# Optimization experiments

Hardware: AMD Instinct MI355X
Metric: run time of the kernel (lower is better)

Reference implementation:

```python
import jax, jax.numpy as jnp
import numpy as np

CH_IN = 128
HD = 128
HEADS = 4
INNER = HD * HEADS  # 512
N_POINTS = 32768
K = 16
BN_EPS = 1e-5


def setup_inputs() -> dict:
    key = jax.random.key(0)
    ks = jax.random.split(key, 8)
    s = CH_IN ** -0.5
    return {
        "h": jax.random.normal(ks[0], (N_POINTS, K, CH_IN), dtype=jnp.float32),
        "x": jax.random.normal(ks[1], (N_POINTS, CH_IN), dtype=jnp.float32),
        "Wq": jax.random.normal(ks[2], (CH_IN, INNER), dtype=jnp.float32) * s,
        "Wk": jax.random.normal(ks[3], (CH_IN, INNER), dtype=jnp.float32) * s,
        "Wv": jax.random.normal(ks[4], (CH_IN, INNER), dtype=jnp.float32) * s,
        "Wo": jax.random.normal(ks[5], (INNER, CH_IN), dtype=jnp.float32) * (INNER ** -0.5),
        "bo": jnp.zeros((CH_IN,), dtype=jnp.float32),
        "gamma": jnp.ones((HD,), dtype=jnp.float32),
        "beta": jnp.zeros((HD,), dtype=jnp.float32),
    }


def reference(h, x, Wq, Wk, Wv, Wo, bo, gamma, beta):
    n, k, c = h.shape
    scale = c ** -0.5
    # QKV projections (no bias)
    q = (x @ Wq).reshape(n, HEADS, HD)                    # [n,h,d]
    kk = (h @ Wk).reshape(n, k, HEADS, HD)                # [n,K,h,d]
    v = (h @ Wv).reshape(n, k, HEADS, HD)                 # [n,K,h,d]
    # per-point attention scores over K neighbors
    scores = jnp.einsum('nkhd,nhd->nhk', kk, q) * scale   # [n,h,K]
    # FAITHFUL: torch softmax is over a trailing singleton dim -> all ones
    w = jax.nn.softmax(scores[..., None], axis=-1)[..., 0]  # [n,h,K] == 1
    out = jnp.einsum('nkhd,nhk->nhd', v, w).reshape(n, INNER)
    # output projection
    out = out @ Wo + bo                                   # [n, ch_in]
    # BatchNorm1d (training-mode batch stats, biased variance)
    mu = out.mean(axis=0)
    var = out.var(axis=0)
    out = (out - mu) * jax.lax.rsqrt(var + BN_EPS) * gamma + beta
    # ReLU (dropout in eval mode = identity)
    return jax.nn.relu(out)
```

## Files before the change

kernel.cpp:

```cpp
#include <hip/hip_runtime.h>

#define NPTS  32768
#define KNB   16
#define CH    128
#define INNER 512
#define EPS   1e-5f

#define WS_M     0
#define WS_STATS 16384

typedef float f4 __attribute__((ext_vector_type(4)));

__global__ __launch_bounds__(256) void k_wvwo(const float* __restrict__ Wv,
                                              const float* __restrict__ Wo,
                                              float* __restrict__ M,
                                              float* __restrict__ stats) {
    int t  = threadIdx.x;
    if (blockIdx.x == 0) stats[t] = 0.f;
    int id = blockIdx.x * 256 + t;
    int c  = id >> 7;
    int cp = id & 127;
    const float* wvr = Wv + c * INNER;
    float a0 = 0.f, a1 = 0.f, a2 = 0.f, a3 = 0.f;
#pragma unroll 4
    for (int i = 0; i < INNER; i += 4) {
        a0 = fmaf(wvr[i + 0], Wo[(i + 0) * CH + cp], a0);
        a1 = fmaf(wvr[i + 1], Wo[(i + 1) * CH + cp], a1);
        a2 = fmaf(wvr[i + 2], Wo[(i + 2) * CH + cp], a2);
        a3 = fmaf(wvr[i + 3], Wo[(i + 3) * CH + cp], a3);
    }
    M[c * CH + cp] = (a0 + a1) + (a2 + a3);
}

__global__ __launch_bounds__(256) void k_main(const float* __restrict__ h,
                                              const float* __restrict__ Mg,
                                              float* __restrict__ y,
                                              float* __restrict__ stats) {
    __shared__ f4    hs4[32 * 32];
    __shared__ float red[4][2][128];

    const int t  = threadIdx.x;
    const int n0 = blockIdx.x * 32;
    const f4* __restrict__ h4 = (const f4*)h;

#pragma unroll 2
    for (int j = 0; j < 4; ++j) {
        int pi = t + 256 * j;
        int p  = pi >> 5;
        int c4 = pi & 31;
        size_t base = (size_t)(n0 + p) * (KNB * 32) + c4;
        f4 a = __builtin_nontemporal_load(&h4[base]);
#pragma unroll
        for (int k = 1; k < KNB; ++k) {
            f4 v = __builtin_nontemporal_load(&h4[base + (size_t)k * 32]);
            a += v;
        }
        hs4[p * 32 + c4] = a;
    }
    __syncthreads();

    const int w  = t >> 6;
    const int l  = t & 63;
    const int p0 = w * 8;
    float acc0[8] = {0,0,0,0,0,0,0,0};
    float acc1[8] = {0,0,0,0,0,0,0,0};

    for (int cc = 0; cc < 32; ++cc) {
        const int c = 4 * cc;
        float m00 = Mg[(c + 0) * CH + l];
        float m01 = Mg[(c + 1) * CH + l];
        float m02 = Mg[(c + 2) * CH + l];
        float m03 = Mg[(c + 3) * CH + l];
        float m10 = Mg[(c + 0) * CH + 64 + l];
        float m11 = Mg[(c + 1) * CH + 64 + l];
        float m12 = Mg[(c + 2) * CH + 64 + l];
        float m13 = Mg[(c + 3) * CH + 64 + l];
#pragma unroll
        for (int p = 0; p < 8; ++p) {
            f4 hv = hs4[(p0 + p) * 32 + cc];
            acc0[p] = fmaf(hv.x, m00, acc0[p]);
            acc0[p] = fmaf(hv.y, m01, acc0[p]);
            acc0[p] = fmaf(hv.z, m02, acc0[p]);
            acc0[p] = fmaf(hv.w, m03, acc0[p]);
            acc1[p] = fmaf(hv.x, m10, acc1[p]);
            acc1[p] = fmaf(hv.y, m11, acc1[p]);
            acc1[p] = fmaf(hv.z, m12, acc1[p]);
            acc1[p] = fmaf(hv.w, m13, acc1[p]);
        }
    }

    float s0 = 0.f, s1 = 0.f, q0 = 0.f, q1 = 0.f;
#pragma unroll
    for (int p = 0; p < 8; ++p) {
        size_t row = (size_t)(n0 + p0 + p) * CH;
        y[row + l]      = acc0[p];
        y[row + 64 + l] = acc1[p];
        s0 += acc0[p];  q0 = fmaf(acc0[p], acc0[p], q0);
        s1 += acc1[p];  q1 = fmaf(acc1[p], acc1[p], q1);
    }
    red[w][0][l]      = s0;
    red[w][0][64 + l] = s1;
    red[w][1][l]      = q0;
    red[w][1][64 + l] = q1;
    __syncthreads();
    {
        int s = t >> 7, c = t & 127;
        float v = red[0][s][c] + red[1][s][c] + red[2][s][c] + red[3][s][c];
        atomicAdd(&stats[t], v);
    }
}

__global__ __launch_bounds__(256) void k_norm(float* __restrict__ y,
                                              const float* __restrict__ stats,
                                              const float* __restrict__ gamma,
                                              const float* __restrict__ beta) {
    __shared__ float sa[128], sb[128];
    int t = threadIdx.x;
    if (t < 128) {
        float S  = stats[t];
        float Q  = stats[128 + t];
        float mu = S * (1.f / NPTS);
        float var = Q * (1.f / NPTS) - mu * mu;
        float a  = gamma[t] * rsqrtf(var + EPS);
        sa[t] = a;
        sb[t] = beta[t] - mu * a;
    }
    __syncthreads();

    int gid = blockIdx.x * 256 + t;
    f4* y4 = (f4*)y;
    int c0 = (gid & 31) * 4;
    f4 a = { sa[c0], sa[c0 + 1], sa[c0 + 2], sa[c0 + 3] };
    f4 b = { sb[c0], sb[c0 + 1], sb[c0 + 2], sb[c0 + 3] };
#pragma unroll
    for (int i = 0; i < 4; ++i) {
        size_t idx = (size_t)gid + (size_t)i * 262144;
        f4 v = y4[idx];
        v.x = fmaxf(0.f, fmaf(v.x, a.x, b.x));
        v.y = fmaxf(0.f, fmaf(v.y, a.y, b.y));
        v.z = fmaxf(0.f, fmaf(v.z, a.z, b.z));
        v.w = fmaxf(0.f, fmaf(v.w, a.w, b.w));
        y4[idx] = v;
    }
}

extern "C" void kernel_launch(void* const* d_in, const int* in_sizes, int n_in,
                              void* d_out, int out_size, void* d_ws, size_t ws_size,
                              hipStream_t stream) {
    const float* h     = (const float*)d_in[0];
    const float* Wv    = (const float*)d_in[4];
    const float* Wo    = (const float*)d_in[5];
    const float* gamma = (const float*)d_in[7];
    const float* beta  = (const float*)d_in[8];

    float* out   = (float*)d_out;
    float* ws    = (float*)d_ws;
    float* M     = ws + WS_M;
    float* stats = ws + WS_STATS;

    k_wvwo<<<64,   256, 0, stream>>>(Wv, Wo, M, stats);
    k_main<<<1024, 256, 0, stream>>>(h, M, out, stats);
    k_norm<<<1024, 256, 0, stream>>>(out, stats, gamma, beta);
}
```

Before: 412.7 us.

## Fuse projection and BatchNorm into one cooperative kernel with grid sync

Replaces the separate main and normalize kernels with one cooperative kernel of 512 blocks, each handling 64 points. Each block keeps its outputs in registers across a grid-wide sync, then applies BatchNorm and ReLU and writes the final values once. This removes the write-then-reread of the intermediate output and one kernel launch. The costs are a grid barrier, higher register pressure from 32 accumulators per thread, and a dependency on all 512 blocks being co-resident; if the cooperative launch fails, the code falls back to the old two-kernel path.

Measured after the change: 452.5 us. +9.6%, slower.

```diff
diff --git a/kernel.cpp b/kernel.cpp
--- a/kernel.cpp
+++ b/kernel.cpp
@@ -1,10 +1,15 @@
 #include <hip/hip_runtime.h>
+#include <hip/hip_cooperative_groups.h>
+
+namespace cg = cooperative_groups;
 
 #define NPTS  32768
 #define KNB   16
 #define CH    128
 #define INNER 512
 #define EPS   1e-5f
+#define PPB   64
+#define NBLK  (NPTS / PPB)
 
 #define WS_M     0
 #define WS_STATS 16384
@@ -32,6 +37,110 @@
     M[c * CH + cp] = (a0 + a1) + (a2 + a3);
 }
 
+__global__ __launch_bounds__(256, 2) void k_fused(const float* __restrict__ h,
+                                                  const float* __restrict__ Mg,
+                                                  float* __restrict__ y,
+                                                  float* __restrict__ stats,
+                                                  const float* __restrict__ gamma,
+                                                  const float* __restrict__ beta) {
+    __shared__ f4    hs4[PPB * 32];
+    __shared__ float red[4][2][128];
+    __shared__ float sa[128], sb[128];
+
+    const int t  = threadIdx.x;
+    const int n0 = blockIdx.x * PPB;
+    const f4* __restrict__ h4 = (const f4*)h;
+
+#pragma unroll 2
+    for (int j = 0; j < 8; ++j) {
+        int pi = t + 256 * j;
+        int p  = pi >> 5;
+        int c4 = pi & 31;
+        size_t base = (size_t)(n0 + p) * (KNB * 32) + c4;
+        f4 a = __builtin_nontemporal_load(&h4[base]);
+#pragma unroll
+        for (int k = 1; k < KNB; ++k) {
+            f4 v = __builtin_nontemporal_load(&h4[base + (size_t)k * 32]);
+            a += v;
+        }
+        hs4[p * 32 + c4] = a;
+    }
+    __syncthreads();
+
+    const int w  = t >> 6;
+    const int l  = t & 63;
+    const int p0 = w * 16;
+    float acc0[16], acc1[16];
+#pragma unroll
+    for (int p = 0; p < 16; ++p) { acc0[p] = 0.f; acc1[p] = 0.f; }
+
+    for (int cc = 0; cc < 32; ++cc) {
+        const int c = 4 * cc;
+        float m00 = Mg[(c + 0) * CH + l];
+        float m01 = Mg[(c + 1) * CH + l];
+        float m02 = Mg[(c + 2) * CH + l];
+        float m03 = Mg[(c + 3) * CH + l];
+        float m10 = Mg[(c + 0) * CH + 64 + l];
+        float m11 = Mg[(c + 1) * CH + 64 + l];
+        float m12 = Mg[(c + 2) * CH + 64 + l];
+        float m13 = Mg[(c + 3) * CH + 64 + l];
+#pragma unroll
+        for (int p = 0; p < 16; ++p) {
+            f4 hv = hs4[(p0 + p) * 32 + cc];
+            acc0[p] = fmaf(hv.x, m00, acc0[p]);
+            acc0[p] = fmaf(hv.y, m01, acc0[p]);
+            acc0[p] = fmaf(hv.z, m02, acc0[p]);
+            acc0[p] = fmaf(hv.w, m03, acc0[p]);
+            acc1[p] = fmaf(hv.x, m10, acc1[p]);
+            acc1[p] = fmaf(hv.y, m11, acc1[p]);
+            acc1[p] = fmaf(hv.z, m12, acc1[p]);
+            acc1[p] = fmaf(hv.w, m13, acc1[p]);
+        }
+    }
+
+    float s0 = 0.f, s1 = 0.f, q0 = 0.f, q1 = 0.f;
+#pragma unroll
+    for (int p = 0; p < 16; ++p) {
+        s0 += acc0[p];  q0 = fmaf(acc0[p], acc0[p], q0);
+        s1 += acc1[p];  q1 = fmaf(acc1[p], acc1[p], q1);
+    }
+    red[w][0][l]      = s0;
+    red[w][0][64 + l] = s1;
+    red[w][1][l]      = q0;
+    red[w][1][64 + l] = q1;
+    __syncthreads();
+    {
+        int s = t >> 7, c = t & 127;
+        float v = red[0][s][c] + red[1][s][c] + red[2][s][c] + red[3][s][c];
+        atomicAdd(&stats[t], v);
+    }
+
+    cg::this_grid().sync();
+
+    if (t < 128) {
+        float S  = __hip_atomic_load(&stats[t],       __ATOMIC_RELAXED,
+                                     __HIP_MEMORY_SCOPE_AGENT);
+        float Q  = __hip_atomic_load(&stats[128 + t], __ATOMIC_RELAXED,
+                                     __HIP_MEMORY_SCOPE_AGENT);
+        float mu  = S * (1.f / NPTS);
+        float var = Q * (1.f / NPTS) - mu * mu;
+        float a   = gamma[t] * rsqrtf(var + EPS);
+        sa[t] = a;
+        sb[t] = beta[t] - mu * a;
+    }
+    __syncthreads();
+
+    float a0 = sa[l], b0 = sb[l], a1 = sa[64 + l], b1 = sb[64 + l];
+#pragma unroll
+    for (int p = 0; p < 16; ++p) {
+        size_t row = (size_t)(n0 + p0 + p) * CH;
+        __builtin_nontemporal_store(fmaxf(0.f, fmaf(acc0[p], a0, b0)),
+                                    &y[row + l]);
+        __builtin_nontemporal_store(fmaxf(0.f, fmaf(acc1[p], a1, b1)),
+                                    &y[row + 64 + l]);
+    }
+}
+
 __global__ __launch_bounds__(256) void k_main(const float* __restrict__ h,
                                               const float* __restrict__ Mg,
                                               float* __restrict__ y,
@@ -158,7 +267,15 @@
     float* M     = ws + WS_M;
     float* stats = ws + WS_STATS;
 
-    k_wvwo<<<64,   256, 0, stream>>>(Wv, Wo, M, stats);
-    k_main<<<1024, 256, 0, stream>>>(h, M, out, stats);
-    k_norm<<<1024, 256, 0, stream>>>(out, stats, gamma, beta);
-}
+    k_wvwo<<<64, 256, 0, stream>>>(Wv, Wo, M, stats);
+
+    void* args[] = { (void*)&h, (void*)&M, (void*)&out, (void*)&stats,
+                     (void*)&gamma, (void*)&beta };
+    hipError_t e = hipLaunchCooperativeKernel((void*)k_fused, dim3(NBLK),
+                                              dim3(256), args, 0, stream);
+    if (e != hipSuccess) {
+        (void)hipGetLastError();
+        k_main<<<1024, 256, 0, stream>>>(h, M, out, stats);
+        k_norm<<<1024, 256, 0, stream>>>(out, stats, gamma, beta);
+    }
+}
```
